# Kernel optimization log

Measured on AMD Instinct MI355X. Metric: run time of the kernel, lower is better.

## Reference

```python
import jax, jax.numpy as jnp
import numpy as np

EMB = 256

def setup_inputs() -> dict:
    key = jax.random.key(0)
    ks = jax.random.split(key, 7)
    c = EMB
    x = jax.random.normal(ks[0], (4, c, 64, 64), dtype=jnp.float32)
    s = 1.0 / np.sqrt(c)
    Wq = jax.random.uniform(ks[1], (c, c), jnp.float32, -s, s)
    bq = jax.random.uniform(ks[2], (c,), jnp.float32, -s, s)
    Wk = jax.random.uniform(ks[3], (c, c), jnp.float32, -s, s)
    bk = jax.random.uniform(ks[4], (c,), jnp.float32, -s, s)
    Wv = jax.random.uniform(ks[5], (c, c), jnp.float32, -s, s)
    bv = jax.random.uniform(ks[6], (c,), jnp.float32, -s, s)
    return {"x": x, "Wq": Wq, "bq": bq, "Wk": Wk, "bk": bk, "Wv": Wv, "bv": bv}

def reference(x, Wq, bq, Wk, bk, Wv, bv):
    b, c, h, w = x.shape
    scale = jnp.sqrt(jnp.float32(c))
    # [b, n, c] tokens, n = h*w
    xt = x.reshape(b, c, h * w).transpose(0, 2, 1)
    q = jnp.einsum('bnc,dc->bnd', xt, Wq) + bq
    k = jnp.einsum('bnc,dc->bnd', xt, Wk) + bk
    v = jnp.einsum('bnc,dc->bnd', xt, Wv) + bv
    dist = jnp.einsum('bnd,bmd->bnm', q, k) / scale  # [b, n, n]
    dist = jax.nn.softmax(dist, axis=-1)
    mem = jnp.einsum('bnm,bmd->bnd', dist, v)  # [b, n, c]
    # Original: permute(0,1,2) is identity, then raw view(b,c,h,w) -> reshape
    return mem.reshape(b, c, h, w)
```

## Files before the change

### kernel.cpp

```cpp
#include <hip/hip_runtime.h>

typedef __attribute__((ext_vector_type(8))) short short8;
typedef __attribute__((ext_vector_type(4))) short short4_t;
typedef __attribute__((ext_vector_type(4))) float float4_t;
typedef __attribute__((ext_vector_type(16))) float float16_t;
typedef __attribute__((ext_vector_type(2))) int int2_t;

#define NTOK 4096
#define CDIM 256
#define BPB (NTOK * CDIM)
#define C1 0.0901684400555602f

__device__ inline float bf2f(short s) {
    return __uint_as_float(((unsigned)(unsigned short)s) << 16);
}
__device__ inline short f2bf(float f) {
    unsigned u = __float_as_uint(f);
    return (short)((u + 0x7fffu + ((u >> 16) & 1u)) >> 16);
}
__device__ inline int cvtpk_bf16(float lo, float hi) {
    int d;
    asm("v_cvt_pk_bf16_f32 %0, %1, %2" : "=v"(d) : "v"(lo), "v"(hi));
    return d;
}
__device__ inline void gl_lds16(const void* g, void* l) {
    __builtin_amdgcn_global_load_lds(
        (const __attribute__((address_space(1))) unsigned int*)g,
        (__attribute__((address_space(3))) unsigned int*)l, 16, 0, 0);
}

__global__ void sniff_dtype(const unsigned* __restrict__ x, int* __restrict__ flag) {
    __shared__ int cnt;
    if (threadIdx.x == 0) cnt = 0;
    __syncthreads();
    int local = 0;
    for (int i = threadIdx.x; i < 1024; i += 256) {
        unsigned e = (x[i] >> 7) & 0xffu;
        if (e >= 100u && e <= 140u) local++;
    }
    atomicAdd(&cnt, local);
    __syncthreads();
    if (threadIdx.x == 0) flag[0] = (cnt >= 512) ? 1 : 0;
}

__global__ __launch_bounds__(256) void wprep(
    const void* __restrict__ Wq, const void* __restrict__ Wk,
    const void* __restrict__ Wv, const int* __restrict__ flag,
    short* __restrict__ Wb)
{
    const int base = (blockIdx.x * 256 + threadIdx.x) * 8;
    const int wsel = base >> 16, off = base & 65535;
    const void* W = (wsel == 0) ? Wq : (wsel == 1) ? Wk : Wv;
    short8 v;
    if (flag[0]) {
        v = *(const short8*)((const short*)W + off);
    } else {
        const float* f = (const float*)W + off;
        float4 a = *(const float4*)f;
        float4 c4 = *(const float4*)(f + 4);
        v[0]=f2bf(a.x);  v[1]=f2bf(a.y);  v[2]=f2bf(a.z);  v[3]=f2bf(a.w);
        v[4]=f2bf(c4.x); v[5]=f2bf(c4.y); v[6]=f2bf(c4.z); v[7]=f2bf(c4.w);
    }
    *(short8*)(Wb + base) = v;
}

template <bool PIN>
__global__ __launch_bounds__(256, 4) void qkv8(
    const void* __restrict__ xv, const short* __restrict__ Wb,
    const void* __restrict__ bq, const void* __restrict__ bk,
    const void* __restrict__ bv,
    const int* __restrict__ flag, int b0,
    short* __restrict__ qbase, short* __restrict__ kbase,
    short* __restrict__ vtbase)
{
    int nt, bl, wsel;
    if (PIN) {
        const int bid = blockIdx.x;
        wsel = bid >> 8;
        const int rem = bid & 255;
        bl = rem & 3; nt = rem >> 2;
    } else { nt = blockIdx.x; wsel = blockIdx.y; bl = blockIdx.z; }
    const int b = b0 + bl;
    const int n0 = nt * 64;
    const int tid = threadIdx.x;
    const int w = tid >> 6, lane = tid & 63, l15 = lane & 15, qd = lane >> 4;
    const int isbf = flag[0];

    __shared__ short obuf[64 * 264];

    short8 af[8];
    {
        const int n = n0 + 16 * w + l15;
        if (isbf) {
            const short* xs = (const short*)xv + (size_t)b * (CDIM * NTOK) + n;
            #pragma unroll
            for (int s = 0; s < 8; ++s) {
                short8 v;
                #pragma unroll
                for (int e = 0; e < 8; ++e)
                    v[e] = xs[(s * 32 + qd * 8 + e) * NTOK];
                af[s] = v;
            }
        } else {
            const float* xf = (const float*)xv + (size_t)b * (CDIM * NTOK) + n;
            #pragma unroll
            for (int s = 0; s < 8; ++s) {
                short8 v;
                #pragma unroll
                for (int e = 0; e < 8; ++e)
                    v[e] = f2bf(xf[(s * 32 + qd * 8 + e) * NTOK]);
                af[s] = v;
            }
        }
    }

    const short* W = Wb + wsel * 65536;
    const void* bp = (wsel == 0) ? bq : (wsel == 1) ? bk : bv;

    short8 wv[8], wn[8];
    {
        const short* wr = W + l15 * 256 + qd * 8;
        #pragma unroll
        for (int s = 0; s < 8; ++s) wv[s] = *(const short8*)(wr + s * 32);
    }
    #pragma unroll 1
    for (int dg = 0; dg < 16; ++dg) {
        const int d = dg * 16 + l15;
        if (dg + 1 < 16) {
            const short* wr = W + (dg * 16 + 16 + l15) * 256 + qd * 8;
            #pragma unroll
            for (int s = 0; s < 8; ++s) wn[s] = *(const short8*)(wr + s * 32);
        }
        float4_t acc = {0.f, 0.f, 0.f, 0.f};
        #pragma unroll
        for (int s = 0; s < 8; ++s)
            acc = __builtin_amdgcn_mfma_f32_16x16x32_bf16(af[s], wv[s], acc, 0, 0, 0);
        const float bias = isbf ? bf2f(((const short*)bp)[d])
                                : ((const float*)bp)[d];
        if (wsel < 2) {
            #pragma unroll
            for (int r = 0; r < 4; ++r)
                obuf[(16 * w + 4 * qd + r) * 264 + d] = f2bf(acc[r] + bias);
        } else {
            #pragma unroll
            for (int r = 0; r < 4; ++r)
                obuf[d * 66 + (16 * w + 4 * qd + r)] = f2bf(acc[r] + bias);
        }
        #pragma unroll
        for (int s = 0; s < 8; ++s) wv[s] = wn[s];
    }
    __syncthreads();

    if (wsel == 0) {
        short* qdst = qbase + (size_t)bl * BPB;
        const int rl = tid >> 2;
        #pragma unroll
        for (int u = 0; u < 8; ++u) {
            const int cc = (tid & 3) + 4 * u;
            short8 vv = *(const short8*)&obuf[rl * 264 + cc * 8];
            *(short8*)(qdst + (size_t)(n0 + rl) * 256 + cc * 8) = vv;
        }
    } else if (wsel == 1) {
        short* kdst = kbase + (size_t)bl * BPB;
        const int rl = tid >> 2;
        const int tile = (n0 + rl) >> 5, rit = rl & 31;
        #pragma unroll
        for (int u = 0; u < 8; ++u) {
            const int ccp = (tid & 3) + 4 * u;
            const int cc  = ccp ^ rit;
            short8 vv = *(const short8*)&obuf[rl * 264 + cc * 8];
            *(short8*)(kdst + (size_t)tile * 8192 + rit * 256 + ccp * 8) = vv;
        }
    } else {
        short* vtdst = vtbase + (size_t)bl * BPB;
        const int d = tid;
        #pragma unroll
        for (int u = 0; u < 8; ++u) {
            short8 vv = *(const short8*)&obuf[d * 66 + u * 8];
            const int tile = (n0 >> 5) + (u >> 2), ck = u & 3;
            const int pos = ((d & 1) * 4 + ck) ^ ((d >> 1) & 7);
            *(short8*)(vtdst + (size_t)tile * 8192 + (d >> 1) * 64 + pos * 8) = vv;
        }
    }
}

__global__ __launch_bounds__(256, 2) void flash13(
    const short* __restrict__ qb, const short* __restrict__ kb,
    const short* __restrict__ vtb,
    float* __restrict__ pO, float* __restrict__ pl)
{
    const int bid = blockIdx.x;
    const int bl = bid & 3, half = (bid >> 2) & 3, qt = bid >> 4;
    const int q0 = qt * 128;
    const int tid = threadIdx.x;
    const int w = tid >> 6, lane = tid & 63, l31 = lane & 31, h = lane >> 5;

    __shared__ __align__(16) char smem[65536];
    short* kbufA = (short*)smem;
    short* vbufA = (short*)(smem + 32768);

    const short* Q  = qb  + (size_t)bl * BPB;
    const char*  Kc = (const char*)(kb  + (size_t)bl * BPB);
    const char*  Vc = (const char*)(vtb + (size_t)bl * BPB);

    short8 qf[16];
    {
        const short* qrow = Q + (size_t)(q0 + 32 * w + l31) * 256 + h * 8;
        #pragma unroll
        for (int s = 0; s < 16; ++s)
            qf[s] = *(const short8*)(qrow + s * 16);
    }

    float16_t oacc[8];
    #pragma unroll
    for (int dt = 0; dt < 8; ++dt)
        #pragma unroll
        for (int r = 0; r < 16; ++r) oacc[dt][r] = 0.f;
    float ll0 = 0.f, ll1 = 0.f, ll2 = 0.f, ll3 = 0.f;

    const int KT0 = half * 32, KT1 = KT0 + 32;

    {
        const char* ks = Kc + ((size_t)KT0 << 14);
        const char* vs = Vc + ((size_t)KT0 << 14);
        char* kd = smem + tid * 16;
        char* vd = smem + 32768 + tid * 16;
        #pragma unroll
        for (int u = 0; u < 4; ++u) {
            gl_lds16(ks + u * 4096 + tid * 16, kd + u * 4096);
            gl_lds16(vs + u * 4096 + tid * 16, vd + u * 4096);
        }
    }

    float16_t se, so;
    #pragma unroll
    for (int r = 0; r < 16; ++r) { se[r] = 0.f; so[r] = 0.f; }
    short8 pa0, pa1;

    #pragma unroll 1
    for (int kt = KT0; kt < KT1; ++kt) {
        if (kt > KT0) {
            #pragma unroll
            for (int r = 0; r < 16; ++r) se[r] = exp2f((se[r] + so[r]) * C1);
            #pragma unroll
            for (int g = 0; g < 4; ++g) {
                ll0 += se[4 * g + 0]; ll1 += se[4 * g + 1];
                ll2 += se[4 * g + 2]; ll3 += se[4 * g + 3];
            }
            {
                int x0 = cvtpk_bf16(se[0], se[1]);
                int y0 = cvtpk_bf16(se[4], se[5]);
                int z0 = cvtpk_bf16(se[2], se[3]);
                int u0 = cvtpk_bf16(se[6], se[7]);
                int2_t r1 = __builtin_amdgcn_permlane32_swap(x0, y0, false, false);
                int2_t r2 = __builtin_amdgcn_permlane32_swap(z0, u0, false, false);
                union { int i[4]; short8 s8; } uu;
                uu.i[0] = r1[0]; uu.i[1] = r2[0]; uu.i[2] = r1[1]; uu.i[3] = r2[1];
                pa0 = uu.s8;
                int x1 = cvtpk_bf16(se[8],  se[9]);
                int y1 = cvtpk_bf16(se[12], se[13]);
                int z1 = cvtpk_bf16(se[10], se[11]);
                int u1 = cvtpk_bf16(se[14], se[15]);
                int2_t r3 = __builtin_amdgcn_permlane32_swap(x1, y1, false, false);
                int2_t r4 = __builtin_amdgcn_permlane32_swap(z1, u1, false, false);
                union { int i[4]; short8 s8; } vv;
                vv.i[0] = r3[0]; vv.i[1] = r4[0]; vv.i[2] = r3[1]; vv.i[3] = r4[1];
                pa1 = vv.s8;
            }
            {
                const short* vprev = vbufA + ((kt + 1) & 1) * 8192;
                __builtin_amdgcn_s_setprio(1);
                #pragma unroll
                for (int dt = 0; dt < 8; ++dt) {
                    const int d = 32 * dt + l31, d2 = d >> 1;
                    {
                        const int pos = (((d & 1) * 4 + h) ^ (d2 & 7));
                        short8 vf = *(const short8*)&vprev[d2 * 64 + pos * 8];
                        oacc[dt] = __builtin_amdgcn_mfma_f32_32x32x16_bf16(pa0, vf, oacc[dt], 0, 0, 0);
                    }
                    {
                        const int pos = (((d & 1) * 4 + 2 + h) ^ (d2 & 7));
                        short8 vf = *(const short8*)&vprev[d2 * 64 + pos * 8];
                        oacc[dt] = __builtin_amdgcn_mfma_f32_32x32x16_bf16(pa1, vf, oacc[dt], 0, 0, 0);
                    }
                }
                __builtin_amdgcn_s_setprio(0);
            }
        }

        asm volatile("s_waitcnt vmcnt(0) lgkmcnt(0)" ::: "memory");
        __builtin_amdgcn_sched_barrier(0);
        __builtin_amdgcn_s_barrier();
        __builtin_amdgcn_sched_barrier(0);

        if (kt + 1 < KT1) {
            const int alt = (kt + 1) & 1;
            const char* ks = Kc + ((size_t)(kt + 1) << 14);
            const char* vs = Vc + ((size_t)(kt + 1) << 14);
            char* kd = smem + alt * 16384 + tid * 16;
            char* vd = smem + 32768 + alt * 16384 + tid * 16;
            #pragma unroll
            for (int u = 0; u < 4; ++u) {
                gl_lds16(ks + u * 4096 + tid * 16, kd + u * 4096);
                gl_lds16(vs + u * 4096 + tid * 16, vd + u * 4096);
            }
        }

        {
            const short* kcur = kbufA + (kt & 1) * 8192;
            #pragma unroll
            for (int r = 0; r < 16; ++r) { se[r] = 0.f; so[r] = 0.f; }
            __builtin_amdgcn_s_setprio(1);
            #pragma unroll
            for (int j = 0; j < 8; ++j) {
                short8 ka = *(const short8*)
                    &kcur[l31 * 256 + (((4 * j + h) ^ l31) * 8)];
                se = __builtin_amdgcn_mfma_f32_32x32x16_bf16(ka, qf[2 * j], se, 0, 0, 0);
                short8 kb2 = *(const short8*)
                    &kcur[l31 * 256 + (((4 * j + 2 + h) ^ l31) * 8)];
                so = __builtin_amdgcn_mfma_f32_32x32x16_bf16(kb2, qf[2 * j + 1], so, 0, 0, 0);
            }
            __builtin_amdgcn_s_setprio(0);
        }
    }

    {
        #pragma unroll
        for (int r = 0; r < 16; ++r) se[r] = exp2f((se[r] + so[r]) * C1);
        #pragma unroll
        for (int g = 0; g < 4; ++g) {
            ll0 += se[4 * g + 0]; ll1 += se[4 * g + 1];
            ll2 += se[4 * g + 2]; ll3 += se[4 * g + 3];
        }
        int x0 = cvtpk_bf16(se[0], se[1]);
        int y0 = cvtpk_bf16(se[4], se[5]);
        int z0 = cvtpk_bf16(se[2], se[3]);
        int u0 = cvtpk_bf16(se[6], se[7]);
        int2_t r1 = __builtin_amdgcn_permlane32_swap(x0, y0, false, false);
        int2_t r2 = __builtin_amdgcn_permlane32_swap(z0, u0, false, false);
        union { int i[4]; short8 s8; } uu;
        uu.i[0] = r1[0]; uu.i[1] = r2[0]; uu.i[2] = r1[1]; uu.i[3] = r2[1];
        pa0 = uu.s8;
        int x1 = cvtpk_bf16(se[8],  se[9]);
        int y1 = cvtpk_bf16(se[12], se[13]);
        int z1 = cvtpk_bf16(se[10], se[11]);
        int u1 = cvtpk_bf16(se[14], se[15]);
        int2_t r3 = __builtin_amdgcn_permlane32_swap(x1, y1, false, false);
        int2_t r4 = __builtin_amdgcn_permlane32_swap(z1, u1, false, false);
        union { int i[4]; short8 s8; } vv;
        vv.i[0] = r3[0]; vv.i[1] = r4[0]; vv.i[2] = r3[1]; vv.i[3] = r4[1];
        pa1 = vv.s8;

        const short* vlast = vbufA + ((KT1 - 1) & 1) * 8192;
        #pragma unroll
        for (int dt = 0; dt < 8; ++dt) {
            const int d = 32 * dt + l31, d2 = d >> 1;
            {
                const int pos = (((d & 1) * 4 + h) ^ (d2 & 7));
                short8 vf = *(const short8*)&vlast[d2 * 64 + pos * 8];
                oacc[dt] = __builtin_amdgcn_mfma_f32_32x32x16_bf16(pa0, vf, oacc[dt], 0, 0, 0);
            }
            {
                const int pos = (((d & 1) * 4 + 2 + h) ^ (d2 & 7));
                short8 vf = *(const short8*)&vlast[d2 * 64 + pos * 8];
                oacc[dt] = __builtin_amdgcn_mfma_f32_32x32x16_bf16(pa1, vf, oacc[dt], 0, 0, 0);
            }
        }
    }

    const size_t idx = (size_t)(bl * 32 + qt) * 4 + half;
    {
        float v2 = (ll0 + ll1) + (ll2 + ll3);
        v2 += __shfl_xor(v2, 32, 64);
        if (h == 0) pl[idx * 128 + 32 * w + l31] = v2;
    }
    float* po = pO + idx * 32768;
    #pragma unroll
    for (int dt = 0; dt < 8; ++dt) {
        #pragma unroll
        for (int r = 0; r < 16; ++r) {
            const int qrow = 32 * w + (r & 3) + 8 * (r >> 2) + 4 * h;
            po[qrow * 256 + 32 * dt + l31] = oacc[dt][r];
        }
    }
}

__global__ __launch_bounds__(256) void combine4(
    const float* __restrict__ pO, const float* __restrict__ pl,
    const int* __restrict__ flag, void* __restrict__ outv)
{
    const int tid = threadIdx.x, w = tid >> 6, lane = tid & 63;
    const int isbf = flag[0];
    #pragma unroll 1
    for (int st = 0; st < 16; ++st) {
        const int row = blockIdx.x * 64 + st * 4 + w;
        const int bl = row >> 12, n = row & 4095;
        const int qt = n >> 7, prow = n & 127;
        const size_t bidx = (size_t)(bl * 32 + qt) * 4;
        const float* P0 = pO + bidx * 32768 + prow * 256 + lane * 4;
        float4 a = *(const float4*)P0;
        float4 b = *(const float4*)(P0 + 32768);
        float4 c = *(const float4*)(P0 + 65536);
        float4 d = *(const float4*)(P0 + 98304);
        const float inv = 1.0f /
            (pl[(bidx + 0) * 128 + prow] + pl[(bidx + 1) * 128 + prow] +
             pl[(bidx + 2) * 128 + prow] + pl[(bidx + 3) * 128 + prow]);
        float4 r;
        r.x = (a.x + b.x + c.x + d.x) * inv;
        r.y = (a.y + b.y + c.y + d.y) * inv;
        r.z = (a.z + b.z + c.z + d.z) * inv;
        r.w = (a.w + b.w + c.w + d.w) * inv;
        const size_t o = (size_t)row * 256 + lane * 4;
        if (isbf) {
            short4_t pk;
            pk[0] = f2bf(r.x); pk[1] = f2bf(r.y);
            pk[2] = f2bf(r.z); pk[3] = f2bf(r.w);
            *(short4_t*)((short*)outv + o) = pk;
        } else {
            *(float4*)((float*)outv + o) = r;
        }
    }
}

template <bool PIN, bool SPLIT>
__global__ __launch_bounds__(256, 2) void flash12(
    int b0, const short* __restrict__ qb, const short* __restrict__ kb,
    const short* __restrict__ vtb, const int* __restrict__ flag,
    void* __restrict__ outv, float* __restrict__ pO, float* __restrict__ pl)
{
    int qt, bl, half;
    if (SPLIT) {
        const int bid = blockIdx.x;
        bl = (bid >> 1) & 3; half = bid & 1; qt = bid >> 3;
    } else if (PIN) {
        bl = blockIdx.x & 3; qt = blockIdx.x >> 2; half = 0;
    } else { qt = blockIdx.x; bl = blockIdx.z; half = 0; }

    const int b = b0 + bl;
    const int q0 = qt * 64;
    const int tid = threadIdx.x;
    const int w = tid >> 6, lane = tid & 63, l31 = lane & 31, h = lane >> 5;
    const int wi = w & 1, wh = w >> 1;

    __shared__ __align__(16) char smem[67584];
    short* kbufA = (short*)smem;
    short* vbufA = (short*)(smem + 32768);
    float* lbuf  = (float*)(smem + 66560);

    const short* Q  = qb  + (size_t)bl * BPB;
    const char*  Kc = (const char*)(kb  + (size_t)bl * BPB);
    const char*  Vc = (const char*)(vtb + (size_t)bl * BPB);

    short8 qf[16];
    {
        const short* qrow = Q + (size_t)(q0 + 32 * wh + l31) * 256 + h * 8;
        #pragma unroll
        for (int s = 0; s < 16; ++s)
            qf[s] = *(const short8*)(qrow + s * 16);
    }

    float16_t oacc[4];
    #pragma unroll
    for (int dt = 0; dt < 4; ++dt)
        #pragma unroll
        for (int r = 0; r < 16; ++r) oacc[dt][r] = 0.f;
    float ll0 = 0.f, ll1 = 0.f, ll2 = 0.f, ll3 = 0.f;

    const int KT0 = SPLIT ? half * 64 : 0;
    const int KT1 = KT0 + (SPLIT ? 64 : 128);

    {
        const char* ks = Kc + ((size_t)KT0 << 14);
        const char* vs = Vc + ((size_t)KT0 << 14);
        char* kd = smem + tid * 16;
        char* vd = smem + 32768 + tid * 16;
        #pragma unroll
        for (int u = 0; u < 4; ++u) {
            gl_lds16(ks + u * 4096 + tid * 16, kd + u * 4096);
            gl_lds16(vs + u * 4096 + tid * 16, vd + u * 4096);
        }
    }
    __syncthreads();

    short8 pa0 = {0,0,0,0,0,0,0,0}, pa1 = {0,0,0,0,0,0,0,0};

    #pragma unroll 1
    for (int kt = KT0; kt < KT1; ++kt) {
        short* kcur  = kbufA + (kt & 1) * 8192;
        short* vprev = vbufA + ((kt + 1) & 1) * 8192;

        if (kt + 1 < KT1) {
            const char* ks = Kc + ((size_t)(kt + 1) << 14);
            char* kd = smem + (((kt + 1) & 1) << 14) + tid * 16;
            #pragma unroll
            for (int u = 0; u < 4; ++u)
                gl_lds16(ks + u * 4096 + tid * 16, kd + u * 4096);
        }

        float16_t se, so;
        #pragma unroll
        for (int r = 0; r < 16; ++r) { se[r] = 0.f; so[r] = 0.f; }
        #pragma unroll
        for (int j = 0; j < 8; ++j) {
            short8 ka = *(const short8*)
                &kcur[l31 * 256 + (((4 * j + h) ^ l31) * 8)];
            se = __builtin_amdgcn_mfma_f32_32x32x16_bf16(ka, qf[2 * j], se, 0, 0, 0);
            short8 kb2 = *(const short8*)
                &kcur[l31 * 256 + (((4 * j + 2 + h) ^ l31) * 8)];
            so = __builtin_amdgcn_mfma_f32_32x32x16_bf16(kb2, qf[2 * j + 1], so, 0, 0, 0);
        }

        if (kt > KT0) {
            #pragma unroll
            for (int dt = 0; dt < 4; ++dt) {
                const int d = 128 * wi + 32 * dt + l31, d2 = d >> 1;
                {
                    const int pos = (((d & 1) * 4 + h) ^ (d2 & 7));
                    short8 vf = *(const short8*)&vprev[d2 * 64 + pos * 8];
                    oacc[dt] = __builtin_amdgcn_mfma_f32_32x32x16_bf16(pa0, vf, oacc[dt], 0, 0, 0);
                }
                {
                    const int pos = (((d & 1) * 4 + 2 + h) ^ (d2 & 7));
                    short8 vf = *(const short8*)&vprev[d2 * 64 + pos * 8];
                    oacc[dt] = __builtin_amdgcn_mfma_f32_32x32x16_bf16(pa1, vf, oacc[dt], 0, 0, 0);
                }
            }
        }

        asm volatile("s_waitcnt lgkmcnt(0)" ::: "memory");
        __builtin_amdgcn_sched_barrier(0);
        __builtin_amdgcn_s_barrier();
        __builtin_amdgcn_sched_barrier(0);

        if (kt + 1 < KT1) {
            const char* vs = Vc + ((size_t)(kt + 1) << 14);
            char* vd = smem + 32768 + (((kt + 1) & 1) << 14) + tid * 16;
            #pragma unroll
            for (int u = 0; u < 4; ++u)
                gl_lds16(vs + u * 4096 + tid * 16, vd + u * 4096);
        }

        float pf[16];
        #pragma unroll
        for (int r = 0; r < 16; ++r) pf[r] = exp2f((se[r] + so[r]) * C1);
        #pragma unroll
        for (int g = 0; g < 4; ++g) {
            ll0 += pf[4 * g + 0]; ll1 += pf[4 * g + 1];
            ll2 += pf[4 * g + 2]; ll3 += pf[4 * g + 3];
        }
        {
            int x0 = cvtpk_bf16(pf[0], pf[1]);
            int y0 = cvtpk_bf16(pf[4], pf[5]);
            int z0 = cvtpk_bf16(pf[2], pf[3]);
            int u0 = cvtpk_bf16(pf[6], pf[7]);
            int2_t r1 = __builtin_amdgcn_permlane32_swap(x0, y0, false, false);
            int2_t r2 = __builtin_amdgcn_permlane32_swap(z0, u0, false, false);
            union { int i[4]; short8 s8; } uu;
            uu.i[0] = r1[0]; uu.i[1] = r2[0]; uu.i[2] = r1[1]; uu.i[3] = r2[1];
            pa0 = uu.s8;
            int x1 = cvtpk_bf16(pf[8],  pf[9]);
            int y1 = cvtpk_bf16(pf[12], pf[13]);
            int z1 = cvtpk_bf16(pf[10], pf[11]);
            int u1 = cvtpk_bf16(pf[14], pf[15]);
            int2_t r3 = __builtin_amdgcn_permlane32_swap(x1, y1, false, false);
            int2_t r4 = __builtin_amdgcn_permlane32_swap(z1, u1, false, false);
            union { int i[4]; short8 s8; } vv;
            vv.i[0] = r3[0]; vv.i[1] = r4[0]; vv.i[2] = r3[1]; vv.i[3] = r4[1];
            pa1 = vv.s8;
        }

        __syncthreads();
    }

    {
        short* vlast = vbufA + 8192;
        #pragma unroll
        for (int dt = 0; dt < 4; ++dt) {
            const int d = 128 * wi + 32 * dt + l31, d2 = d >> 1;
            {
                const int pos = (((d & 1) * 4 + h) ^ (d2 & 7));
                short8 vf = *(const short8*)&vlast[d2 * 64 + pos * 8];
                oacc[dt] = __builtin_amdgcn_mfma_f32_32x32x16_bf16(pa0, vf, oacc[dt], 0, 0, 0);
            }
            {
                const int pos = (((d & 1) * 4 + 2 + h) ^ (d2 & 7));
                short8 vf = *(const short8*)&vlast[d2 * 64 + pos * 8];
                oacc[dt] = __builtin_amdgcn_mfma_f32_32x32x16_bf16(pa1, vf, oacc[dt], 0, 0, 0);
            }
        }
    }

    {
        float v2 = (ll0 + ll1) + (ll2 + ll3);
        v2 += __shfl_xor(v2, 32, 64);
        if (h == 0 && wi == 0) lbuf[32 * wh + l31] = v2;
    }

    if (SPLIT) {
        const size_t pidx = (size_t)(bl * 64 + qt) * 2 + half;
        float* po = pO + pidx * 16384;
        #pragma unroll
        for (int dt = 0; dt < 4; ++dt) {
            const int dim = 128 * wi + 32 * dt + l31;
            #pragma unroll
            for (int r = 0; r < 16; ++r) {
                const int qrow = 32 * wh + (r & 3) + 8 * (r >> 2) + 4 * h;
                po[qrow * 256 + dim] = oacc[dt][r];
            }
        }
        __syncthreads();
        if (tid < 64) pl[pidx * 64 + tid] = lbuf[tid];
    } else {
        __syncthreads();
        float* obuf = (float*)smem;
        #pragma unroll
        for (int dt = 0; dt < 4; ++dt) {
            const int dim = 128 * wi + 32 * dt + l31;
            #pragma unroll
            for (int r = 0; r < 16; ++r) {
                const int qrow = 32 * wh + (r & 3) + 8 * (r >> 2) + 4 * h;
                obuf[qrow * 260 + dim] = oacc[dt][r];
            }
        }
        __syncthreads();
        {
            const int row = tid >> 2, q4 = (tid & 3) * 64;
            const float inv = 1.0f / lbuf[row];
            const float* src = obuf + row * 260 + q4;
            const size_t o = (size_t)(b * NTOK + q0 + row) * 256 + q4;
            if (flag[0]) {
                short* op = (short*)outv;
                #pragma unroll
                for (int g = 0; g < 4; ++g) {
                    float4 a  = *(const float4*)(src + g * 8);
                    float4 c4 = *(const float4*)(src + g * 8 + 4);
                    short8 pk;
                    pk[0]=f2bf(a.x*inv);  pk[1]=f2bf(a.y*inv);
                    pk[2]=f2bf(a.z*inv);  pk[3]=f2bf(a.w*inv);
                    pk[4]=f2bf(c4.x*inv); pk[5]=f2bf(c4.y*inv);
                    pk[6]=f2bf(c4.z*inv); pk[7]=f2bf(c4.w*inv);
                    *(short8*)(op + o + g * 8) = pk;
                }
            } else {
                float* op = (float*)outv;
                #pragma unroll
                for (int g = 0; g < 16; ++g) {
                    float4 a = *(const float4*)(src + g * 4);
                    a.x *= inv; a.y *= inv; a.z *= inv; a.w *= inv;
                    *(float4*)(op + o + g * 4) = a;
                }
            }
        }
    }
}

__global__ __launch_bounds__(256) void combine2(
    const float* __restrict__ pO, const float* __restrict__ pl,
    const int* __restrict__ flag, void* __restrict__ outv)
{
    const int tile = blockIdx.x, tid = threadIdx.x;
    const int row = tid >> 2, seg = (tid & 3) * 64;
    const float* A = pO + (size_t)tile * 32768 + row * 256 + seg;
    const float* B = A + 16384;
    const float inv = 1.0f / (pl[tile * 128 + row] + pl[tile * 128 + 64 + row]);
    const size_t o = ((size_t)tile * 64 + row) * 256 + seg;
    if (flag[0]) {
        short* op = (short*)outv;
        #pragma unroll
        for (int g = 0; g < 8; ++g) {
            float4 a  = *(const float4*)(A + g * 8);
            float4 a2 = *(const float4*)(A + g * 8 + 4);
            float4 c  = *(const float4*)(B + g * 8);
            float4 c2 = *(const float4*)(B + g * 8 + 4);
            short8 pk;
            pk[0]=f2bf((a.x+c.x)*inv);   pk[1]=f2bf((a.y+c.y)*inv);
            pk[2]=f2bf((a.z+c.z)*inv);   pk[3]=f2bf((a.w+c.w)*inv);
            pk[4]=f2bf((a2.x+c2.x)*inv); pk[5]=f2bf((a2.y+c2.y)*inv);
            pk[6]=f2bf((a2.z+c2.z)*inv); pk[7]=f2bf((a2.w+c2.w)*inv);
            *(short8*)(op + o + g * 8) = pk;
        }
    } else {
        float* op = (float*)outv;
        #pragma unroll
        for (int g = 0; g < 16; ++g) {
            float4 a = *(const float4*)(A + g * 4);
            float4 c = *(const float4*)(B + g * 4);
            a.x = (a.x + c.x) * inv; a.y = (a.y + c.y) * inv;
            a.z = (a.z + c.z) * inv; a.w = (a.w + c.w) * inv;
            *(float4*)(op + o + g * 4) = a;
        }
    }
}

extern "C" void kernel_launch(void* const* d_in, const int* in_sizes, int n_in,
                              void* d_out, int out_size, void* d_ws, size_t ws_size,
                              hipStream_t stream)
{
    const size_t HDR = 256;
    const size_t WBB = 393216;
    const size_t TB  = (size_t)BPB * 2;
    const size_t OFF_K = HDR + WBB;
    const size_t need_prim = OFF_K + 12 * TB;
    const size_t PO2 = 33554432;
    const size_t need_s2 = need_prim + PO2 + 131072;
    const size_t PO4 = 67108864;
    const size_t need_s4 = need_prim + PO4 + 262144;

    int*   flag = (int*)d_ws;
    short* Wb   = (short*)((char*)d_ws + HDR);

    sniff_dtype<<<1, 256, 0, stream>>>((const unsigned*)d_in[0], flag);
    wprep<<<96, 256, 0, stream>>>(d_in[1], d_in[3], d_in[5], flag, Wb);

    if (ws_size >= need_prim) {
        short* kbase  = (short*)((char*)d_ws + OFF_K);
        short* vtbase = kbase  + 4 * (size_t)BPB;
        short* qbase  = vtbase + 4 * (size_t)BPB;
        qkv8<true><<<dim3(768, 1, 1), 256, 0, stream>>>(
            d_in[0], Wb, d_in[2], d_in[4], d_in[6], flag, 0,
            qbase, kbase, vtbase);
        if (ws_size >= need_s4) {
            float* pO = (float*)((char*)d_ws + need_prim);
            float* pl = (float*)((char*)d_ws + need_prim + PO4);
            flash13<<<dim3(512, 1, 1), 256, 0, stream>>>(
                qbase, kbase, vtbase, pO, pl);
            combine4<<<dim3(256, 1, 1), 256, 0, stream>>>(pO, pl, flag, d_out);
        } else if (ws_size >= need_s2) {
            float* pO = (float*)((char*)d_ws + need_prim);
            float* pl = (float*)((char*)d_ws + need_prim + PO2);
            flash12<true, true><<<dim3(512, 1, 1), 256, 0, stream>>>(
                0, qbase, kbase, vtbase, flag, d_out, pO, pl);
            combine2<<<dim3(256, 1, 1), 256, 0, stream>>>(pO, pl, flag, d_out);
        } else {
            flash12<true, false><<<dim3(256, 1, 1), 256, 0, stream>>>(
                0, qbase, kbase, vtbase, flag, d_out, nullptr, nullptr);
        }
        return;
    }

    int nb = 4;
    while (nb > 1 && ws_size < OFF_K + (size_t)nb * 3 * TB) nb--;
    short* kbase  = (short*)((char*)d_ws + OFF_K);
    short* vtbase = kbase + (size_t)nb * BPB;
    short* qbase  = vtbase + (size_t)nb * BPB;

    for (int b0 = 0; b0 < 4; b0 += nb) {
        const int nbc = (4 - b0) < nb ? (4 - b0) : nb;
        qkv8<false><<<dim3(64, 3, nbc), 256, 0, stream>>>(
            d_in[0], Wb, d_in[2], d_in[4], d_in[6], flag, b0,
            qbase, kbase, vtbase);
        flash12<false, false><<<dim3(64, 1, nbc), 256, 0, stream>>>(
            b0, qbase, kbase, vtbase, flag, d_out, nullptr, nullptr);
    }
}
```

Before: 224.7 us.

## Merge dtype sniff into weight prep, split QKV accumulators, drop setprio, widen combine grid

Folds the dtype-detection kernel into the weight-conversion kernel so one launch disappears. The QKV projection now uses two independent MFMA accumulator chains to shorten the dependency chain. The s_setprio hints are removed from the flash13 inner loops. The combine4 kernel runs twice as many blocks with half the rows each. The unused split flash12 path and combine2 are deleted. Every block of the merged kernel now re-reads the same 1024 input words to sniff the dtype, a small amount of redundant work.

```diff
diff --git a/kernel.cpp b/kernel.cpp
--- a/kernel.cpp
+++ b/kernel.cpp
@@ -29,30 +29,30 @@
         (__attribute__((address_space(3))) unsigned int*)l, 16, 0, 0);
 }
 
-__global__ void sniff_dtype(const unsigned* __restrict__ x, int* __restrict__ flag) {
-    __shared__ int cnt;
-    if (threadIdx.x == 0) cnt = 0;
+__global__ __launch_bounds__(256) void wprep2(
+    const void* __restrict__ Wq, const void* __restrict__ Wk,
+    const void* __restrict__ Wv, const unsigned* __restrict__ x,
+    int* __restrict__ flag, short* __restrict__ Wb)
+{
+    __shared__ int cs;
+    if (threadIdx.x == 0) cs = 0;
     __syncthreads();
     int local = 0;
     for (int i = threadIdx.x; i < 1024; i += 256) {
         unsigned e = (x[i] >> 7) & 0xffu;
         if (e >= 100u && e <= 140u) local++;
     }
-    atomicAdd(&cnt, local);
+    atomicAdd(&cs, local);
     __syncthreads();
-    if (threadIdx.x == 0) flag[0] = (cnt >= 512) ? 1 : 0;
-}
-
-__global__ __launch_bounds__(256) void wprep(
-    const void* __restrict__ Wq, const void* __restrict__ Wk,
-    const void* __restrict__ Wv, const int* __restrict__ flag,
-    short* __restrict__ Wb)
-{
+    const int isbf = (cs >= 512) ? 1 : 0;
+
+    if (blockIdx.x == 0 && threadIdx.x == 0) flag[0] = isbf;
+
     const int base = (blockIdx.x * 256 + threadIdx.x) * 8;
     const int wsel = base >> 16, off = base & 65535;
     const void* W = (wsel == 0) ? Wq : (wsel == 1) ? Wk : Wv;
     short8 v;
-    if (flag[0]) {
+    if (isbf) {
         v = *(const short8*)((const short*)W + off);
     } else {
         const float* f = (const float*)W + off;
@@ -65,7 +65,7 @@
 }
 
 template <bool PIN>
-__global__ __launch_bounds__(256, 4) void qkv8(
+__global__ __launch_bounds__(256, 4) void qkv8b(
     const void* __restrict__ xv, const short* __restrict__ Wb,
     const void* __restrict__ bq, const void* __restrict__ bk,
     const void* __restrict__ bv,
@@ -131,20 +131,23 @@
             #pragma unroll
             for (int s = 0; s < 8; ++s) wn[s] = *(const short8*)(wr + s * 32);
         }
-        float4_t acc = {0.f, 0.f, 0.f, 0.f};
-        #pragma unroll
-        for (int s = 0; s < 8; ++s)
-            acc = __builtin_amdgcn_mfma_f32_16x16x32_bf16(af[s], wv[s], acc, 0, 0, 0);
+        float4_t ae = {0.f, 0.f, 0.f, 0.f};
+        float4_t ao = {0.f, 0.f, 0.f, 0.f};
+        #pragma unroll
+        for (int s = 0; s < 4; ++s) {
+            ae = __builtin_amdgcn_mfma_f32_16x16x32_bf16(af[2*s],   wv[2*s],   ae, 0, 0, 0);
+            ao = __builtin_amdgcn_mfma_f32_16x16x32_bf16(af[2*s+1], wv[2*s+1], ao, 0, 0, 0);
+        }
         const float bias = isbf ? bf2f(((const short*)bp)[d])
                                 : ((const float*)bp)[d];
         if (wsel < 2) {
             #pragma unroll
             for (int r = 0; r < 4; ++r)
-                obuf[(16 * w + 4 * qd + r) * 264 + d] = f2bf(acc[r] + bias);
+                obuf[(16 * w + 4 * qd + r) * 264 + d] = f2bf(ae[r] + ao[r] + bias);
         } else {
             #pragma unroll
             for (int r = 0; r < 4; ++r)
-                obuf[d * 66 + (16 * w + 4 * qd + r)] = f2bf(acc[r] + bias);
+                obuf[d * 66 + (16 * w + 4 * qd + r)] = f2bf(ae[r] + ao[r] + bias);
         }
         #pragma unroll
         for (int s = 0; s < 8; ++s) wv[s] = wn[s];
@@ -269,7 +272,6 @@
             }
             {
                 const short* vprev = vbufA + ((kt + 1) & 1) * 8192;
-                __builtin_amdgcn_s_setprio(1);
                 #pragma unroll
                 for (int dt = 0; dt < 8; ++dt) {
                     const int d = 32 * dt + l31, d2 = d >> 1;
@@ -284,7 +286,6 @@
                         oacc[dt] = __builtin_amdgcn_mfma_f32_32x32x16_bf16(pa1, vf, oacc[dt], 0, 0, 0);
                     }
                 }
-                __builtin_amdgcn_s_setprio(0);
             }
         }
 
@@ -310,7 +311,6 @@
             const short* kcur = kbufA + (kt & 1) * 8192;
             #pragma unroll
             for (int r = 0; r < 16; ++r) { se[r] = 0.f; so[r] = 0.f; }
-            __builtin_amdgcn_s_setprio(1);
             #pragma unroll
             for (int j = 0; j < 8; ++j) {
                 short8 ka = *(const short8*)
@@ -320,7 +320,6 @@
                     &kcur[l31 * 256 + (((4 * j + 2 + h) ^ l31) * 8)];
                 so = __builtin_amdgcn_mfma_f32_32x32x16_bf16(kb2, qf[2 * j + 1], so, 0, 0, 0);
             }
-            __builtin_amdgcn_s_setprio(0);
         }
     }
 
@@ -351,7 +350,7 @@
         vv.i[0] = r3[0]; vv.i[1] = r4[0]; vv.i[2] = r3[1]; vv.i[3] = r4[1];
         pa1 = vv.s8;
 
-        const short* vlast = vbufA + ((KT1 - 1) & 1) * 8192;
+        const short* vlast = vbufA + 8192;
         #pragma unroll
         for (int dt = 0; dt < 8; ++dt) {
             const int d = 32 * dt + l31, d2 = d >> 1;
@@ -392,8 +391,8 @@
     const int tid = threadIdx.x, w = tid >> 6, lane = tid & 63;
     const int isbf = flag[0];
     #pragma unroll 1
-    for (int st = 0; st < 16; ++st) {
-        const int row = blockIdx.x * 64 + st * 4 + w;
+    for (int st = 0; st < 8; ++st) {
+        const int row = blockIdx.x * 32 + st * 4 + w;
         const int bl = row >> 12, n = row & 4095;
         const int qt = n >> 7, prow = n & 127;
         const size_t bidx = (size_t)(bl * 32 + qt) * 4;
@@ -422,19 +421,15 @@
     }
 }
 
-template <bool PIN, bool SPLIT>
+template <bool PIN>
 __global__ __launch_bounds__(256, 2) void flash12(
     int b0, const short* __restrict__ qb, const short* __restrict__ kb,
     const short* __restrict__ vtb, const int* __restrict__ flag,
-    void* __restrict__ outv, float* __restrict__ pO, float* __restrict__ pl)
+    void* __restrict__ outv)
 {
-    int qt, bl, half;
-    if (SPLIT) {
-        const int bid = blockIdx.x;
-        bl = (bid >> 1) & 3; half = bid & 1; qt = bid >> 3;
-    } else if (PIN) {
-        bl = blockIdx.x & 3; qt = blockIdx.x >> 2; half = 0;
-    } else { qt = blockIdx.x; bl = blockIdx.z; half = 0; }
+    int qt, bl;
+    if (PIN) { bl = blockIdx.x & 3; qt = blockIdx.x >> 2; }
+    else     { qt = blockIdx.x; bl = blockIdx.z; }
 
     const int b = b0 + bl;
     const int q0 = qt * 64;
@@ -466,12 +461,9 @@
         for (int r = 0; r < 16; ++r) oacc[dt][r] = 0.f;
     float ll0 = 0.f, ll1 = 0.f, ll2 = 0.f, ll3 = 0.f;
 
-    const int KT0 = SPLIT ? half * 64 : 0;
-    const int KT1 = KT0 + (SPLIT ? 64 : 128);
-
-    {
-        const char* ks = Kc + ((size_t)KT0 << 14);
-        const char* vs = Vc + ((size_t)KT0 << 14);
+    {
+        const char* ks = Kc;
+        const char* vs = Vc;
         char* kd = smem + tid * 16;
         char* vd = smem + 32768 + tid * 16;
         #pragma unroll
@@ -485,11 +477,11 @@
     short8 pa0 = {0,0,0,0,0,0,0,0}, pa1 = {0,0,0,0,0,0,0,0};
 
     #pragma unroll 1
-    for (int kt = KT0; kt < KT1; ++kt) {
+    for (int kt = 0; kt < 128; ++kt) {
         short* kcur  = kbufA + (kt & 1) * 8192;
         short* vprev = vbufA + ((kt + 1) & 1) * 8192;
 
-        if (kt + 1 < KT1) {
+        if (kt + 1 < 128) {
             const char* ks = Kc + ((size_t)(kt + 1) << 14);
             char* kd = smem + (((kt + 1) & 1) << 14) + tid * 16;
             #pragma unroll
@@ -510,7 +502,7 @@
             so = __builtin_amdgcn_mfma_f32_32x32x16_bf16(kb2, qf[2 * j + 1], so, 0, 0, 0);
         }
 
-        if (kt > KT0) {
+        if (kt > 0) {
             #pragma unroll
             for (int dt = 0; dt < 4; ++dt) {
                 const int d = 128 * wi + 32 * dt + l31, d2 = d >> 1;
@@ -532,7 +524,7 @@
         __builtin_amdgcn_s_barrier();
         __builtin_amdgcn_sched_barrier(0);
 
-        if (kt + 1 < KT1) {
+        if (kt + 1 < 128) {
             const char* vs = Vc + ((size_t)(kt + 1) << 14);
             char* vd = smem + 32768 + (((kt + 1) & 1) << 14) + tid * 16;
             #pragma unroll
@@ -596,98 +588,44 @@
         if (h == 0 && wi == 0) lbuf[32 * wh + l31] = v2;
     }
 
-    if (SPLIT) {
-        const size_t pidx = (size_t)(bl * 64 + qt) * 2 + half;
-        float* po = pO + pidx * 16384;
-        #pragma unroll
-        for (int dt = 0; dt < 4; ++dt) {
-            const int dim = 128 * wi + 32 * dt + l31;
-            #pragma unroll
-            for (int r = 0; r < 16; ++r) {
-                const int qrow = 32 * wh + (r & 3) + 8 * (r >> 2) + 4 * h;
-                po[qrow * 256 + dim] = oacc[dt][r];
-            }
-        }
-        __syncthreads();
-        if (tid < 64) pl[pidx * 64 + tid] = lbuf[tid];
-    } else {
-        __syncthreads();
-        float* obuf = (float*)smem;
-        #pragma unroll
-        for (int dt = 0; dt < 4; ++dt) {
-            const int dim = 128 * wi + 32 * dt + l31;
-            #pragma unroll
-            for (int r = 0; r < 16; ++r) {
-                const int qrow = 32 * wh + (r & 3) + 8 * (r >> 2) + 4 * h;
-                obuf[qrow * 260 + dim] = oacc[dt][r];
-            }
-        }
-        __syncthreads();
-        {
-            const int row = tid >> 2, q4 = (tid & 3) * 64;
-            const float inv = 1.0f / lbuf[row];
-            const float* src = obuf + row * 260 + q4;
-            const size_t o = (size_t)(b * NTOK + q0 + row) * 256 + q4;
-            if (flag[0]) {
-                short* op = (short*)outv;
-                #pragma unroll
-                for (int g = 0; g < 4; ++g) {
-                    float4 a  = *(const float4*)(src + g * 8);
-                    float4 c4 = *(const float4*)(src + g * 8 + 4);
-                    short8 pk;
-                    pk[0]=f2bf(a.x*inv);  pk[1]=f2bf(a.y*inv);
-                    pk[2]=f2bf(a.z*inv);  pk[3]=f2bf(a.w*inv);
-                    pk[4]=f2bf(c4.x*inv); pk[5]=f2bf(c4.y*inv);
-                    pk[6]=f2bf(c4.z*inv); pk[7]=f2bf(c4.w*inv);
-                    *(short8*)(op + o + g * 8) = pk;
-                }
-            } else {
-                float* op = (float*)outv;
-                #pragma unroll
-                for (int g = 0; g < 16; ++g) {
-                    float4 a = *(const float4*)(src + g * 4);
-                    a.x *= inv; a.y *= inv; a.z *= inv; a.w *= inv;
-                    *(float4*)(op + o + g * 4) = a;
-                }
-            }
-        }
-    }
-}
-
-__global__ __launch_bounds__(256) void combine2(
-    const float* __restrict__ pO, const float* __restrict__ pl,
-    const int* __restrict__ flag, void* __restrict__ outv)
-{
-    const int tile = blockIdx.x, tid = threadIdx.x;
-    const int row = tid >> 2, seg = (tid & 3) * 64;
-    const float* A = pO + (size_t)tile * 32768 + row * 256 + seg;
-    const float* B = A + 16384;
-    const float inv = 1.0f / (pl[tile * 128 + row] + pl[tile * 128 + 64 + row]);
-    const size_t o = ((size_t)tile * 64 + row) * 256 + seg;
-    if (flag[0]) {
-        short* op = (short*)outv;
-        #pragma unroll
-        for (int g = 0; g < 8; ++g) {
-            float4 a  = *(const float4*)(A + g * 8);
-            float4 a2 = *(const float4*)(A + g * 8 + 4);
-            float4 c  = *(const float4*)(B + g * 8);
-            float4 c2 = *(const float4*)(B + g * 8 + 4);
-            short8 pk;
-            pk[0]=f2bf((a.x+c.x)*inv);   pk[1]=f2bf((a.y+c.y)*inv);
-            pk[2]=f2bf((a.z+c.z)*inv);   pk[3]=f2bf((a.w+c.w)*inv);
-            pk[4]=f2bf((a2.x+c2.x)*inv); pk[5]=f2bf((a2.y+c2.y)*inv);
-            pk[6]=f2bf((a2.z+c2.z)*inv); pk[7]=f2bf((a2.w+c2.w)*inv);
-            *(short8*)(op + o + g * 8) = pk;
-        }
-    } else {
-        float* op = (float*)outv;
-        #pragma unroll
-        for (int g = 0; g < 16; ++g) {
-            float4 a = *(const float4*)(A + g * 4);
-            float4 c = *(const float4*)(B + g * 4);
-            a.x = (a.x + c.x) * inv; a.y = (a.y + c.y) * inv;
-            a.z = (a.z + c.z) * inv; a.w = (a.w + c.w) * inv;
-            *(float4*)(op + o + g * 4) = a;
+    __syncthreads();
+    float* obuf = (float*)smem;
+    #pragma unroll
+    for (int dt = 0; dt < 4; ++dt) {
+        const int dim = 128 * wi + 32 * dt + l31;
+        #pragma unroll
+        for (int r = 0; r < 16; ++r) {
+            const int qrow = 32 * wh + (r & 3) + 8 * (r >> 2) + 4 * h;
+            obuf[qrow * 260 + dim] = oacc[dt][r];
+        }
+    }
+    __syncthreads();
+    {
+        const int row = tid >> 2, q4 = (tid & 3) * 64;
+        const float inv = 1.0f / lbuf[row];
+        const float* src = obuf + row * 260 + q4;
+        const size_t o = (size_t)(b * NTOK + q0 + row) * 256 + q4;
+        if (flag[0]) {
+            short* op = (short*)outv;
+            #pragma unroll
+            for (int g = 0; g < 4; ++g) {
+                float4 a  = *(const float4*)(src + g * 8);
+                float4 c4 = *(const float4*)(src + g * 8 + 4);
+                short8 pk;
+                pk[0]=f2bf(a.x*inv);  pk[1]=f2bf(a.y*inv);
+                pk[2]=f2bf(a.z*inv);  pk[3]=f2bf(a.w*inv);
+                pk[4]=f2bf(c4.x*inv); pk[5]=f2bf(c4.y*inv);
+                pk[6]=f2bf(c4.z*inv); pk[7]=f2bf(c4.w*inv);
+                *(short8*)(op + o + g * 8) = pk;
+            }
+        } else {
+            float* op = (float*)outv;
+            #pragma unroll
+            for (int g = 0; g < 16; ++g) {
+                float4 a = *(const float4*)(src + g * 4);
+                a.x *= inv; a.y *= inv; a.z *= inv; a.w *= inv;
+                *(float4*)(op + o + g * 4) = a;
+            }
         }
     }
 }
@@ -696,27 +634,25 @@
                               void* d_out, int out_size, void* d_ws, size_t ws_size,
                               hipStream_t stream)
 {
-    const size_t HDR = 256;
+    const size_t HDR = 1024;
     const size_t WBB = 393216;
     const size_t TB  = (size_t)BPB * 2;
     const size_t OFF_K = HDR + WBB;
     const size_t need_prim = OFF_K + 12 * TB;
-    const size_t PO2 = 33554432;
-    const size_t need_s2 = need_prim + PO2 + 131072;
     const size_t PO4 = 67108864;
     const size_t need_s4 = need_prim + PO4 + 262144;
 
     int*   flag = (int*)d_ws;
     short* Wb   = (short*)((char*)d_ws + HDR);
 
-    sniff_dtype<<<1, 256, 0, stream>>>((const unsigned*)d_in[0], flag);
-    wprep<<<96, 256, 0, stream>>>(d_in[1], d_in[3], d_in[5], flag, Wb);
+    wprep2<<<96, 256, 0, stream>>>(
+        d_in[1], d_in[3], d_in[5], (const unsigned*)d_in[0], flag, Wb);
 
     if (ws_size >= need_prim) {
         short* kbase  = (short*)((char*)d_ws + OFF_K);
         short* vtbase = kbase  + 4 * (size_t)BPB;
         short* qbase  = vtbase + 4 * (size_t)BPB;
-        qkv8<true><<<dim3(768, 1, 1), 256, 0, stream>>>(
+        qkv8b<true><<<dim3(768, 1, 1), 256, 0, stream>>>(
             d_in[0], Wb, d_in[2], d_in[4], d_in[6], flag, 0,
             qbase, kbase, vtbase);
         if (ws_size >= need_s4) {
@@ -724,16 +660,10 @@
             float* pl = (float*)((char*)d_ws + need_prim + PO4);
             flash13<<<dim3(512, 1, 1), 256, 0, stream>>>(
                 qbase, kbase, vtbase, pO, pl);
-            combine4<<<dim3(256, 1, 1), 256, 0, stream>>>(pO, pl, flag, d_out);
-        } else if (ws_size >= need_s2) {
-            float* pO = (float*)((char*)d_ws + need_prim);
-            float* pl = (float*)((char*)d_ws + need_prim + PO2);
-            flash12<true, true><<<dim3(512, 1, 1), 256, 0, stream>>>(
-                0, qbase, kbase, vtbase, flag, d_out, pO, pl);
-            combine2<<<dim3(256, 1, 1), 256, 0, stream>>>(pO, pl, flag, d_out);
+            combine4<<<dim3(512, 1, 1), 256, 0, stream>>>(pO, pl, flag, d_out);
         } else {
-            flash12<true, false><<<dim3(256, 1, 1), 256, 0, stream>>>(
-                0, qbase, kbase, vtbase, flag, d_out, nullptr, nullptr);
+            flash12<true><<<dim3(256, 1, 1), 256, 0, stream>>>(
+                0, qbase, kbase, vtbase, flag, d_out);
         }
         return;
     }
@@ -746,10 +676,10 @@
 
     for (int b0 = 0; b0 < 4; b0 += nb) {
         const int nbc = (4 - b0) < nb ? (4 - b0) : nb;
-        qkv8<false><<<dim3(64, 3, nbc), 256, 0, stream>>>(
+        qkv8b<false><<<dim3(64, 3, nbc), 256, 0, stream>>>(
             d_in[0], Wb, d_in[2], d_in[4], d_in[6], flag, b0,
             qbase, kbase, vtbase);
-        flash12<false, false><<<dim3(64, 1, nbc), 256, 0, stream>>>(
-            b0, qbase, kbase, vtbase, flag, d_out, nullptr, nullptr);
-    }
-}
+        flash12<false><<<dim3(64, 1, nbc), 256, 0, stream>>>(
+            b0, qbase, kbase, vtbase, flag, d_out);
+    }
+}
```

New measurement: 223.0 us. About the same (-0.7%).
